# Kernel tuning notes

Hardware: AMD Instinct MI355X
Metric: run time of the kernel (lower is better)

## Reference

```python
import jax, jax.numpy as jnp
import numpy as np
import math

NUM_HEADS = 16
ROPE_BASE = 10000.0
SLIDING_WINDOW = 512  # note: original triu-then-tril composition makes the mask empty (no-op)


def _rope_cos_sin(seq_len, head_dim, dtype):
    inv_freq = 1.0 / (ROPE_BASE ** (jnp.arange(0, head_dim, 2, dtype=jnp.float32) / head_dim))
    t = jnp.arange(seq_len, dtype=jnp.float32)
    freqs = t[:, None] * inv_freq[None, :]          # [S, D/2]
    emb = jnp.concatenate([freqs, freqs], axis=-1)  # [S, D]
    # reshape to broadcast over [B, S, H, D]
    return jnp.cos(emb)[None, :, None, :].astype(dtype), jnp.sin(emb)[None, :, None, :].astype(dtype)


def _rotate_half(x):
    x1, x2 = jnp.split(x, 2, axis=-1)
    return jnp.concatenate([-x2, x1], axis=-1)


def setup_inputs() -> dict:
    key = jax.random.key(0)
    ks = jax.random.split(key, 9)
    B, S, E = 2, 2048, 2048
    sc = 1.0 / math.sqrt(E)
    return {
        "hidden_states": jax.random.normal(ks[0], (B, S, E), dtype=jnp.float32),
        "Wq": jax.random.normal(ks[1], (E, E), dtype=jnp.float32) * sc,
        "bq": jax.random.normal(ks[2], (E,), dtype=jnp.float32) * 0.01,
        "Wk": jax.random.normal(ks[3], (E, E), dtype=jnp.float32) * sc,
        "bk": jax.random.normal(ks[4], (E,), dtype=jnp.float32) * 0.01,
        "Wv": jax.random.normal(ks[5], (E, E), dtype=jnp.float32) * sc,
        "bv": jax.random.normal(ks[6], (E,), dtype=jnp.float32) * 0.01,
        "Wo": jax.random.normal(ks[7], (E, E), dtype=jnp.float32) * sc,
        "bo": jax.random.normal(ks[8], (E,), dtype=jnp.float32) * 0.01,
    }


def reference(hidden_states, Wq, bq, Wk, bk, Wv, bv, Wo, bo):
    B, S, E = hidden_states.shape
    H = NUM_HEADS
    D = E // H
    q = (hidden_states @ Wq.T + bq).reshape(B, S, H, D)
    k = (hidden_states @ Wk.T + bk).reshape(B, S, H, D)
    v = (hidden_states @ Wv.T + bv).reshape(B, S, H, D)

    cos, sin = _rope_cos_sin(S, D, q.dtype)
    q = q * cos + _rotate_half(q) * sin
    k = k * cos + _rotate_half(k) * sin

    scale = 1.0 / math.sqrt(D)
    scores = jnp.einsum("bqhd,bkhd->bhqk", q, k) * scale  # [B,H,S,S]
    # Faithful to source: triu(ones, +w) followed by tril(..., -w) is empty -> mask is a no-op.
    attn = jax.nn.softmax(scores, axis=-1)
    out = jnp.einsum("bhqk,bkhd->bqhd", attn, v).reshape(B, S, E)
    return out @ Wo.T + bo
```

## Files before the change

kernel.cpp:

```cpp
#include <hip/hip_runtime.h>
#include <hip/hip_bf16.h>

#define B_ 2
#define S_ 2048
#define E_ 2048
#define H_ 16
#define D_ 128
#define M_ (B_*S_)
#define NQKV_ (3*E_)

typedef __attribute__((ext_vector_type(8))) short bf16x8;
typedef __attribute__((ext_vector_type(4))) float f32x4;
typedef __attribute__((ext_vector_type(4))) unsigned short u16x4;
typedef __attribute__((ext_vector_type(2))) unsigned u32x2;

__device__ __forceinline__ unsigned short f2bf(float f) {
  union { float f; unsigned u; } v; v.f = f;
  unsigned r = v.u + 0x7fffu + ((v.u >> 16) & 1u);
  return (unsigned short)(r >> 16);
}
__device__ __forceinline__ float bf2f(unsigned short h) {
  union { unsigned u; float f; } v; v.u = ((unsigned)h) << 16;
  return v.f;
}

__device__ __forceinline__ void gload_lds16(const void* g, void* l) {
  __builtin_amdgcn_global_load_lds(
      (const __attribute__((address_space(1))) unsigned*)g,
      (__attribute__((address_space(3))) unsigned*)l, 16, 0, 0);
}

__global__ __launch_bounds__(256) void prep_kernel(
    const float* __restrict__ hs,
    const float* __restrict__ Wq, const float* __restrict__ Wk, const float* __restrict__ Wv,
    const float* __restrict__ Wo,
    const float* __restrict__ bq, const float* __restrict__ bk, const float* __restrict__ bv,
    unsigned short* __restrict__ hsb, unsigned short* __restrict__ Wqkv,
    unsigned short* __restrict__ Wob, float* __restrict__ biasqkv,
    float* __restrict__ cosT, float* __restrict__ sinT)
{
  const int seg = blockIdx.y;
  const int t0 = blockIdx.x * 256 + threadIdx.x;
  const int stride = gridDim.x * 256;
  if (seg == 0) {
    const int n = (M_*E_)/4;
    for (int i = t0; i < n; i += stride) {
      f32x4 v = ((const f32x4*)hs)[i];
      u16x4 o; o[0]=f2bf(v[0]); o[1]=f2bf(v[1]); o[2]=f2bf(v[2]); o[3]=f2bf(v[3]);
      ((u16x4*)hsb)[i] = o;
    }
  } else if (seg == 1) {
    const int n = (3*E_*E_)/4;
    for (int i = t0; i < n; i += stride) {
      int e4 = i << 2;
      int r = e4 >> 11;
      int k = e4 & 2047;
      const float* src = (r < E_) ? (Wq + ((size_t)r << 11) + k)
                       : (r < 2*E_) ? (Wk + ((size_t)(r - E_) << 11) + k)
                       : (Wv + ((size_t)(r - 2*E_) << 11) + k);
      f32x4 v = *(const f32x4*)src;
      u16x4 o; o[0]=f2bf(v[0]); o[1]=f2bf(v[1]); o[2]=f2bf(v[2]); o[3]=f2bf(v[3]);
      ((u16x4*)Wqkv)[i] = o;
    }
  } else if (seg == 2) {
    const int n = (E_*E_)/4;
    for (int i = t0; i < n; i += stride) {
      f32x4 v = ((const f32x4*)Wo)[i];
      u16x4 o; o[0]=f2bf(v[0]); o[1]=f2bf(v[1]); o[2]=f2bf(v[2]); o[3]=f2bf(v[3]);
      ((u16x4*)Wob)[i] = o;
    }
  } else if (seg == 3) {
    for (int i = t0; i < NQKV_; i += stride)
      biasqkv[i] = (i < E_) ? bq[i] : (i < 2*E_) ? bk[i - E_] : bv[i - 2*E_];
  } else {
    for (int i = t0; i < S_*64; i += stride) {
      int j = i & 63, s = i >> 6;
      float inv = exp2f(-(float)j * (13.287712379549449f / 64.0f));
      float ang = (float)s * inv;
      cosT[i] = cosf(ang);
      sinT[i] = sinf(ang);
    }
  }
}

#define STGA(BUFP, TKT, KS) do { \
    unsigned short* dst_ = lds + (BUFP)*24576 + (KS)*4096; \
    const unsigned short* src_ = Abase + (TKT)*64 + (KS)*32; \
    int cc_ = tid; int row_ = cc_ >> 2, c2_ = cc_ & 3; \
    int sc_ = c2_ ^ ((row_ >> 1) & 3); \
    gload_lds16(src_ + (size_t)row_*K + sc_*8, (char*)dst_ + cc_*16); \
  } while(0)

#define STGB(BUFP, TKT, KS) do { \
    unsigned short* dst_ = lds + (BUFP)*24576 + 8192 + (KS)*8192; \
    const unsigned short* src_ = Bbase + (TKT)*64 + (KS)*32; \
    _Pragma("unroll") \
    for (int j_ = 0; j_ < 2; ++j_) { \
      int cc_ = (j_ << 9) + tid; int row_ = cc_ >> 2, c2_ = cc_ & 3; \
      int sc_ = c2_ ^ ((row_ >> 1) & 3); \
      gload_lds16(src_ + (size_t)row_*K + sc_*8, (char*)dst_ + cc_*16); \
    } } while(0)

#define PHA(KS, BUF, ISSUE, WAITV) do { \
    { const unsigned short* Ab_ = lds + (BUF)*24576 + (KS)*4096; \
      _Pragma("unroll") \
      for (int j_ = 0; j_ < 4; ++j_) { \
        int row_ = wr*64 + j_*16 + l15; \
        af[j_] = *(const bf16x8*)(Ab_ + row_*32 + ((l4 ^ ((row_>>1)&3)) << 3)); } \
      const unsigned short* Bb_ = lds + (BUF)*24576 + 8192 + (KS)*8192; \
      _Pragma("unroll") \
      for (int j_ = 0; j_ < 4; ++j_) { \
        int row_ = wc*64 + j_*16 + l15; \
        bf[j_] = *(const bf16x8*)(Bb_ + row_*32 + ((l4 ^ ((row_>>1)&3)) << 3)); } } \
    ISSUE; \
    __builtin_amdgcn_sched_barrier(0); \
    __builtin_amdgcn_s_barrier(); \
    asm volatile("s_waitcnt lgkmcnt(0)" ::: "memory"); \
    __builtin_amdgcn_sched_barrier(0); \
    __builtin_amdgcn_s_setprio(1); \
    _Pragma("unroll") \
    for (int mm_ = 0; mm_ < 4; ++mm_) \
      _Pragma("unroll") \
      for (int nn_ = 0; nn_ < 4; ++nn_) \
        acc[mm_][nn_] = __builtin_amdgcn_mfma_f32_16x16x32_bf16(af[mm_], bf[nn_], acc[mm_][nn_], 0,0,0); \
    __builtin_amdgcn_s_setprio(0); \
    WAITV; \
    __builtin_amdgcn_s_barrier(); \
  } while(0)

template<int OUT_F32>
__global__ __launch_bounds__(512, 2) void gemmA(
    const unsigned short* __restrict__ A,
    const unsigned short* __restrict__ Bm,
    const float* __restrict__ bias,
    void* __restrict__ Cv,
    int M, int N, int K)
{
  __shared__ __align__(16) unsigned short lds[73728];
  const int tid = threadIdx.x;
  const int lane = tid & 63;
  const int w = tid >> 6;
  const int wr = w >> 2, wc = w & 3;
  const int l15 = lane & 15, l4 = lane >> 4;

  const int ntile = N >> 8;
  int wg = blockIdx.x;
  const int cpx = gridDim.x >> 3;
  wg = (wg & 7) * cpx + (wg >> 3);
  const int tm = wg / ntile, tn = wg % ntile;

  const unsigned short* Abase = A + ((size_t)tm*128)*K;
  const unsigned short* Bbase = Bm + ((size_t)tn*256)*K;

  f32x4 acc[4][4] = {};
  bf16x8 af[4], bf[4];

  const int NT = K >> 6;

  STGA(0,0,0); STGB(0,0,0); STGA(0,0,1); STGB(0,0,1);
  STGA(1,1,0); STGB(1,1,0); STGA(1,1,1); STGB(1,1,1);
  __builtin_amdgcn_sched_barrier(0);
  asm volatile("s_waitcnt vmcnt(6)" ::: "memory");
  __builtin_amdgcn_s_barrier();
  __builtin_amdgcn_sched_barrier(0);

  int bufc = 0, bufn = 2;
  for (int i = 0; i < NT; ++i) {
    const bool st = (i + 2 < NT);
    const bool more = (i + 1 < NT);
    PHA(0, bufc, if (st) { STGA(bufn, i+2, 0); STGB(bufn, i+2, 0); }, );
    PHA(1, bufc, if (st) { STGA(bufn, i+2, 1); STGB(bufn, i+2, 1); },
        if (st) { asm volatile("s_waitcnt vmcnt(6)" ::: "memory"); }
        else if (more) { asm volatile("s_waitcnt vmcnt(0)" ::: "memory"); });
    bufc = (bufc + 1 == 3) ? 0 : bufc + 1;
    bufn = (bufn + 1 == 3) ? 0 : bufn + 1;
  }

  #pragma unroll
  for (int mt = 0; mt < 4; ++mt) {
    #pragma unroll
    for (int nt = 0; nt < 4; ++nt) {
      int colg = tn*256 + wc*64 + nt*16 + l15;
      float bvv = bias[colg];
      #pragma unroll
      for (int r = 0; r < 4; ++r) {
        int rowg = tm*128 + wr*64 + mt*16 + l4*4 + r;
        float v = acc[mt][nt][r] + bvv;
        if (OUT_F32) ((float*)Cv)[(size_t)rowg*N + colg] = v;
        else ((unsigned short*)Cv)[(size_t)rowg*N + colg] = f2bf(v);
      }
    }
  }
}

__global__ __launch_bounds__(256) void rope_kernel(
    unsigned short* __restrict__ qkv, const float* __restrict__ cosT, const float* __restrict__ sinT)
{
  int t = blockIdx.x*256 + threadIdx.x;
  int i  = t & 63;
  int h  = (t >> 6) & 15;
  int m  = t >> 10;
  int s  = m & (S_-1);
  float c = cosT[s*64 + i], sn = sinT[s*64 + i];
  const float scale = 0.08838834764831845f * 1.4426950408889634f;
  size_t base = (size_t)m*NQKV_ + h*128;
  float q1 = bf2f(qkv[base+i]), q2 = bf2f(qkv[base+64+i]);
  qkv[base+i]    = f2bf((q1*c - q2*sn)*scale);
  qkv[base+64+i] = f2bf((q2*c + q1*sn)*scale);
  size_t kb = base + E_;
  float k1 = bf2f(qkv[kb+i]), k2 = bf2f(qkv[kb+64+i]);
  qkv[kb+i]    = f2bf(k1*c - k2*sn);
  qkv[kb+64+i] = f2bf(k2*c + k1*sn);
}

__global__ __launch_bounds__(256) void transv_kernel(
    const unsigned short* __restrict__ qkv, unsigned short* __restrict__ Vt)
{
  __shared__ unsigned short t[32][33];
  int bid = blockIdx.x;
  int st = bid & 63;
  int dt = (bid >> 6) & 3;
  int bh = bid >> 8;
  int b = bh >> 4, h = bh & 15;
  int tx = threadIdx.x & 31, ty = threadIdx.x >> 5;
  #pragma unroll
  for (int j = 0; j < 4; ++j) {
    int r = ty + j*8;
    t[r][tx] = qkv[(size_t)(b*S_ + st*32 + r)*NQKV_ + 2*E_ + h*128 + dt*32 + tx];
  }
  __syncthreads();
  #pragma unroll
  for (int j = 0; j < 4; ++j) {
    int r = ty + j*8;
    Vt[((size_t)bh*D_ + dt*32 + r)*S_ + st*32 + tx] = t[tx][r];
  }
}

__global__ __launch_bounds__(256, 2) void attn_kernel(
    const unsigned short* __restrict__ qkv, const unsigned short* __restrict__ Vt,
    unsigned short* __restrict__ Ao)
{
  __shared__ unsigned short lK[64*128];
  __shared__ unsigned short lV[128*64];
  __shared__ __align__(16) unsigned short lP[4*32*64];
  int bid = blockIdx.x;
  bid = (bid & 7)*64 + (bid >> 3);
  const int qt = bid & 15;
  const int bh = bid >> 4;
  const int b = bh >> 4, h = bh & 15;
  const int tid = threadIdx.x, lane = tid & 63, w = tid >> 6;
  const int l15 = lane & 15, l4 = lane >> 4;

  bf16x8 qf[2][4];
  #pragma unroll
  for (int g = 0; g < 2; ++g) {
    const int qrow = qt*128 + w*32 + g*16 + l15;
    const unsigned short* qp = qkv + (size_t)(b*S_ + qrow)*NQKV_ + h*128 + l4*8;
    #pragma unroll
    for (int f = 0; f < 4; ++f) qf[g][f] = *(const bf16x8*)(qp + f*32);
  }

  f32x4 O[2][8];
  #pragma unroll
  for (int g = 0; g < 2; ++g)
    #pragma unroll
    for (int i = 0; i < 8; ++i) O[g][i] = (f32x4){0.f,0.f,0.f,0.f};
  float mx[2] = {-1e30f,-1e30f}, lsum[2] = {0.f,0.f};

  unsigned short* myP = lP + w*(32*64);
  const int ksw = (l15 & 7) << 3;
  const size_t kbase = (size_t)b*S_*NQKV_ + E_ + (size_t)h*128;
  const size_t vbase = (size_t)bh*D_*S_;

  for (int kt = 0; kt < S_; kt += 64) {
    #pragma unroll
    for (int i = 0; i < 4; ++i) {
      int cc = i*256 + tid;
      int row = cc >> 4, col = cc & 15;
      int scol = col ^ (row & 7);
      gload_lds16(qkv + kbase + (size_t)(kt + row)*NQKV_ + scol*8, (char*)lK + cc*16);
    }
    #pragma unroll
    for (int i = 0; i < 4; ++i) {
      int cc = i*256 + tid;
      int row = cc >> 3, col = cc & 7;
      int scol = col ^ ((row & 7) ^ ((row >> 3) & 7));
      gload_lds16(Vt + vbase + (size_t)row*S_ + kt + scol*8, (char*)lV + cc*16);
    }
    asm volatile("s_waitcnt vmcnt(0)" ::: "memory");
    __syncthreads();

    f32x4 sfr[2][4];
    #pragma unroll
    for (int nf = 0; nf < 4; ++nf) {
      f32x4 s0 = (f32x4){0.f,0.f,0.f,0.f};
      f32x4 s1 = (f32x4){0.f,0.f,0.f,0.f};
      #pragma unroll
      for (int ks = 0; ks < 4; ++ks) {
        int row = nf*16 + l15;
        int ch = (ks*4 + l4) ^ (row & 7);
        bf16x8 kf = *(const bf16x8*)(lK + row*128 + ch*8);
        s0 = __builtin_amdgcn_mfma_f32_16x16x32_bf16(kf, qf[0][ks], s0, 0, 0, 0);
        s1 = __builtin_amdgcn_mfma_f32_16x16x32_bf16(kf, qf[1][ks], s1, 0, 0, 0);
      }
      sfr[0][nf] = s0; sfr[1][nf] = s1;
    }

    float vm[2];
    #pragma unroll
    for (int g = 0; g < 2; ++g) {
      float v = -1e30f;
      #pragma unroll
      for (int nf = 0; nf < 4; ++nf)
        #pragma unroll
        for (int r = 0; r < 4; ++r) v = fmaxf(v, sfr[g][nf][r]);
      v = fmaxf(v, __shfl_xor(v, 16, 64));
      v = fmaxf(v, __shfl_xor(v, 32, 64));
      vm[g] = v;
    }

    if (__any((vm[0] > mx[0] + 8.0f) || (vm[1] > mx[1] + 8.0f))) {
      #pragma unroll
      for (int g = 0; g < 2; ++g) {
        float mn = fmaxf(mx[g], vm[g]);
        float al = __builtin_amdgcn_exp2f(mx[g] - mn);
        mx[g] = mn;
        lsum[g] *= al;
        #pragma unroll
        for (int r = 0; r < 4; ++r) {
          float ar = __shfl(al, (lane & 48) + l4*4 + r, 64);
          #pragma unroll
          for (int df = 0; df < 8; ++df) O[g][df][r] *= ar;
        }
      }
    }

    #pragma unroll
    for (int g = 0; g < 2; ++g) {
      float ps = 0.f;
      #pragma unroll
      for (int nf = 0; nf < 4; ++nf) {
        #pragma unroll
        for (int r = 0; r < 4; ++r) {
          float p = __builtin_amdgcn_exp2f(sfr[g][nf][r] - mx[g]);
          sfr[g][nf][r] = p;
          ps += p;
        }
      }
      ps += __shfl_xor(ps, 16, 64);
      ps += __shfl_xor(ps, 32, 64);
      lsum[g] += ps;
    }

    #pragma unroll
    for (int g = 0; g < 2; ++g) {
      #pragma unroll
      for (int nf = 0; nf < 4; ++nf) {
        unsigned lo = (unsigned)f2bf(sfr[g][nf][0]) | ((unsigned)f2bf(sfr[g][nf][1]) << 16);
        unsigned hi = (unsigned)f2bf(sfr[g][nf][2]) | ((unsigned)f2bf(sfr[g][nf][3]) << 16);
        int k0 = (nf*16 + l4*4) ^ ksw;
        u32x2 val; val[0] = lo; val[1] = hi;
        *(u32x2*)(myP + (g*16 + l15)*64 + k0) = val;
      }
    }
    asm volatile("s_waitcnt lgkmcnt(0)" ::: "memory");

    #pragma unroll
    for (int ks2 = 0; ks2 < 2; ++ks2) {
      int kk = (ks2*32 + l4*8) ^ ksw;
      bf16x8 pf0 = *(const bf16x8*)(myP + l15*64 + kk);
      bf16x8 pf1 = *(const bf16x8*)(myP + (16 + l15)*64 + kk);
      #pragma unroll
      for (int df = 0; df < 8; ++df) {
        int row = df*16 + l15;
        int ch = (ks2*4 + l4) ^ ((row & 7) ^ ((row >> 3) & 7));
        bf16x8 vf = *(const bf16x8*)(lV + row*64 + ch*8);
        O[0][df] = __builtin_amdgcn_mfma_f32_16x16x32_bf16(pf0, vf, O[0][df], 0, 0, 0);
        O[1][df] = __builtin_amdgcn_mfma_f32_16x16x32_bf16(pf1, vf, O[1][df], 0, 0, 0);
      }
    }
    __syncthreads();
  }

  #pragma unroll
  for (int g = 0; g < 2; ++g) {
    float linv = 1.0f / lsum[g];
    float inv[4];
    #pragma unroll
    for (int r = 0; r < 4; ++r) inv[r] = __shfl(linv, (lane & 48) + l4*4 + r, 64);
    #pragma unroll
    for (int df = 0; df < 8; ++df) {
      int colg = h*128 + df*16 + l15;
      #pragma unroll
      for (int r = 0; r < 4; ++r) {
        int rowg = qt*128 + w*32 + g*16 + l4*4 + r;
        Ao[(size_t)(b*S_ + rowg)*E_ + colg] = f2bf(O[g][df][r] * inv[r]);
      }
    }
  }
}

extern "C" void kernel_launch(void* const* d_in, const int* in_sizes, int n_in,
                              void* d_out, int out_size, void* d_ws, size_t ws_size,
                              hipStream_t stream) {
  const float* hs = (const float*)d_in[0];
  const float* Wq = (const float*)d_in[1];
  const float* bq = (const float*)d_in[2];
  const float* Wk = (const float*)d_in[3];
  const float* bk = (const float*)d_in[4];
  const float* Wv = (const float*)d_in[5];
  const float* bv = (const float*)d_in[6];
  const float* Wo = (const float*)d_in[7];
  const float* bo = (const float*)d_in[8];
  float* out = (float*)d_out;

  char* p = (char*)d_ws;
  auto alloc = [&](size_t bytes) { char* r = p; p += (bytes + 255) & ~(size_t)255; return r; };
  unsigned short* hsb  = (unsigned short*)alloc((size_t)M_*E_*2);
  unsigned short* Wqkv = (unsigned short*)alloc((size_t)NQKV_*E_*2);
  unsigned short* Wob  = (unsigned short*)alloc((size_t)E_*E_*2);
  unsigned short* qkv  = (unsigned short*)alloc((size_t)M_*NQKV_*2);
  unsigned short* Vt   = (unsigned short*)alloc((size_t)B_*H_*D_*S_*2);
  unsigned short* Ao   = (unsigned short*)alloc((size_t)M_*E_*2);
  float* biasqkv = (float*)alloc((size_t)NQKV_*4);
  float* cosT = (float*)alloc((size_t)S_*64*4);
  float* sinT = (float*)alloc((size_t)S_*64*4);

  prep_kernel<<<dim3(2048, 5), 256, 0, stream>>>(hs, Wq, Wk, Wv, Wo, bq, bk, bv,
      hsb, Wqkv, Wob, biasqkv, cosT, sinT);
  gemmA<0><<<dim3((M_/128)*(NQKV_/256)), 512, 0, stream>>>(hsb, Wqkv, biasqkv, qkv, M_, NQKV_, E_);
  rope_kernel<<<dim3((M_*H_*64)/256), 256, 0, stream>>>(qkv, cosT, sinT);
  transv_kernel<<<dim3(B_*H_*(D_/32)*(S_/32)), 256, 0, stream>>>(qkv, Vt);
  attn_kernel<<<dim3(B_*H_*(S_/128)), 256, 0, stream>>>(qkv, Vt, Ao);
  gemmA<1><<<dim3((M_/128)*(E_/256)), 512, 0, stream>>>(Ao, Wob, bo, out, M_, E_, E_);
}
```

Baseline: 298.7 us.

## Add 256x256-tile GEMM for Q/K projection and split V projection

Adds a new GEMM kernel with 256x256 output tiles (each wave computing 128x64) and a double-buffered two-stage K pipeline. It is used for the Q and K projection columns. The V projection goes through the existing 128x256 kernel, called with a separate leading dimension so both write into the shared qkv buffer. Larger tiles raise arithmetic intensity and data reuse per block, but they double accumulator registers, cut the block count to 128 for Q/K, and add an extra kernel launch.

```diff
diff --git a/kernel.cpp b/kernel.cpp
--- a/kernel.cpp
+++ b/kernel.cpp
@@ -79,6 +79,123 @@
       float ang = (float)s * inv;
       cosT[i] = cosf(ang);
       sinT[i] = sinf(ang);
+    }
+  }
+}
+
+#define STAGE8(basePtr, BUF, AB, KS, KT) do { \
+    unsigned short* dst_ = lds + (BUF)*32768 + (AB)*16384 + (KS)*8192; \
+    const unsigned short* src_ = (basePtr) + (KT)*64 + (KS)*32; \
+    _Pragma("unroll") \
+    for (int j_ = 0; j_ < 2; ++j_) { \
+      int cc_ = (j_ << 9) + tid; \
+      int row_ = cc_ >> 2, c2_ = cc_ & 3; \
+      int sc_ = c2_ ^ ((row_ >> 1) & 3); \
+      gload_lds16(src_ + (size_t)row_*K + sc_*8, (char*)dst_ + cc_*16); \
+    } } while(0)
+
+#define LOADA8(MH, KS, BUF) do { \
+    const unsigned short* Ab_ = lds + (BUF)*32768 + (KS)*8192; \
+    _Pragma("unroll") \
+    for (int j_ = 0; j_ < 4; ++j_) { \
+      int row_ = wr*128 + ((MH)*4 + j_)*16 + l15; \
+      af[j_] = *(const bf16x8*)(Ab_ + row_*32 + ((l4 ^ ((row_>>1)&3)) << 3)); \
+    } } while(0)
+
+#define LOADB8(KS, BUF) do { \
+    const unsigned short* Bb_ = lds + (BUF)*32768 + 16384 + (KS)*8192; \
+    _Pragma("unroll") \
+    for (int j_ = 0; j_ < 4; ++j_) { \
+      int row_ = wc*64 + j_*16 + l15; \
+      bf[j_] = *(const bf16x8*)(Bb_ + row_*32 + ((l4 ^ ((row_>>1)&3)) << 3)); \
+    } } while(0)
+
+#define MFMAQ(MH) do { \
+    _Pragma("unroll") \
+    for (int mm_ = 0; mm_ < 4; ++mm_) \
+      _Pragma("unroll") \
+      for (int nn_ = 0; nn_ < 4; ++nn_) \
+        acc[(MH)*4+mm_][nn_] = __builtin_amdgcn_mfma_f32_16x16x32_bf16(af[mm_], bf[nn_], acc[(MH)*4+mm_][nn_], 0,0,0); \
+  } while(0)
+
+#define WVM6 asm volatile("s_waitcnt vmcnt(6)" ::: "memory")
+#define WVM0 asm volatile("s_waitcnt vmcnt(0)" ::: "memory")
+
+#define PHASE(MH, KS, BUF, ISSUE, WAITV) do { \
+    LOADA8(MH, KS, BUF); \
+    if ((MH) == 0) LOADB8(KS, BUF); \
+    ISSUE; \
+    __builtin_amdgcn_sched_barrier(0); \
+    __builtin_amdgcn_s_barrier(); \
+    asm volatile("s_waitcnt lgkmcnt(0)" ::: "memory"); \
+    __builtin_amdgcn_sched_barrier(0); \
+    __builtin_amdgcn_s_setprio(1); \
+    MFMAQ(MH); \
+    __builtin_amdgcn_s_setprio(0); \
+    WAITV; \
+    __builtin_amdgcn_s_barrier(); \
+  } while(0)
+
+__global__ __launch_bounds__(512, 2) void gemm8(
+    const unsigned short* __restrict__ A,
+    const unsigned short* __restrict__ Bm,
+    const float* __restrict__ bias,
+    unsigned short* __restrict__ Cv,
+    int M, int N, int K, int ldc)
+{
+  __shared__ __align__(16) unsigned short lds[65536];
+  const int tid = threadIdx.x;
+  const int lane = tid & 63;
+  const int w = tid >> 6;
+  const int wr = w >> 2, wc = w & 3;
+  const int l15 = lane & 15, l4 = lane >> 4;
+
+  const int ntile = N >> 8;
+  int wg = blockIdx.x;
+  const int cpx = gridDim.x >> 3;
+  wg = (wg & 7) * cpx + (wg >> 3);
+  const int tm = wg / ntile, tn = wg % ntile;
+
+  const unsigned short* Abase = A + ((size_t)tm*256)*K;
+  const unsigned short* Bbase = Bm + ((size_t)tn*256)*K;
+
+  f32x4 acc[8][4] = {};
+  bf16x8 af[4], bf[4];
+
+  const int NITER = K >> 7;
+
+  STAGE8(Bbase, 0, 1, 0, 0); STAGE8(Abase, 0, 0, 0, 0);
+  STAGE8(Bbase, 0, 1, 1, 0); STAGE8(Abase, 0, 0, 1, 0);
+  STAGE8(Bbase, 1, 1, 0, 1); STAGE8(Abase, 1, 0, 0, 1);
+  STAGE8(Bbase, 1, 1, 1, 1);
+  __builtin_amdgcn_sched_barrier(0);
+  WVM6;
+  __builtin_amdgcn_s_barrier();
+
+  for (int i = 0; i < NITER; ++i) {
+    const int t1k = 2*i + 1, t2k = 2*i + 2, t3k = 2*i + 3;
+    const bool nl = (i < NITER - 1);
+    PHASE(0, 0, 0, STAGE8(Abase, 1, 0, 1, t1k), );
+    PHASE(1, 0, 0, if (nl) STAGE8(Bbase, 0, 1, 0, t2k), );
+    PHASE(0, 1, 0, if (nl) STAGE8(Abase, 0, 0, 0, t2k), );
+    PHASE(1, 1, 0, if (nl) STAGE8(Bbase, 0, 1, 1, t2k), if (nl) WVM6; else WVM0);
+    PHASE(0, 0, 1, if (nl) STAGE8(Abase, 0, 0, 1, t2k), );
+    PHASE(1, 0, 1, if (nl) STAGE8(Bbase, 1, 1, 0, t3k), );
+    PHASE(0, 1, 1, if (nl) STAGE8(Abase, 1, 0, 0, t3k), );
+    PHASE(1, 1, 1, if (nl) STAGE8(Bbase, 1, 1, 1, t3k), if (nl) WVM6);
+  }
+
+  #pragma unroll
+  for (int mt = 0; mt < 8; ++mt) {
+    #pragma unroll
+    for (int nt = 0; nt < 4; ++nt) {
+      int colg = tn*256 + wc*64 + nt*16 + l15;
+      float bvv = bias[colg];
+      #pragma unroll
+      for (int r = 0; r < 4; ++r) {
+        int rowg = tm*256 + wr*128 + mt*16 + l4*4 + r;
+        Cv[(size_t)rowg*ldc + colg] = f2bf(acc[mt][nt][r] + bvv);
+      }
     }
   }
 }
@@ -134,7 +251,7 @@
     const unsigned short* __restrict__ Bm,
     const float* __restrict__ bias,
     void* __restrict__ Cv,
-    int M, int N, int K)
+    int M, int N, int K, int ldc)
 {
   __shared__ __align__(16) unsigned short lds[73728];
   const int tid = threadIdx.x;
@@ -186,8 +303,8 @@
       for (int r = 0; r < 4; ++r) {
         int rowg = tm*128 + wr*64 + mt*16 + l4*4 + r;
         float v = acc[mt][nt][r] + bvv;
-        if (OUT_F32) ((float*)Cv)[(size_t)rowg*N + colg] = v;
-        else ((unsigned short*)Cv)[(size_t)rowg*N + colg] = f2bf(v);
+        if (OUT_F32) ((float*)Cv)[(size_t)rowg*ldc + colg] = v;
+        else ((unsigned short*)Cv)[(size_t)rowg*ldc + colg] = f2bf(v);
       }
     }
   }
@@ -428,9 +545,13 @@
 
   prep_kernel<<<dim3(2048, 5), 256, 0, stream>>>(hs, Wq, Wk, Wv, Wo, bq, bk, bv,
       hsb, Wqkv, Wob, biasqkv, cosT, sinT);
-  gemmA<0><<<dim3((M_/128)*(NQKV_/256)), 512, 0, stream>>>(hsb, Wqkv, biasqkv, qkv, M_, NQKV_, E_);
+  gemm8<<<dim3((M_/256)*(2*E_/256)), 512, 0, stream>>>(
+      hsb, Wqkv, biasqkv, qkv, M_, 2*E_, E_, NQKV_);
+  gemmA<0><<<dim3((M_/128)*(E_/256)), 512, 0, stream>>>(
+      hsb, Wqkv + (size_t)2*E_*E_, biasqkv + 2*E_, qkv + 2*E_, M_, E_, E_, NQKV_);
   rope_kernel<<<dim3((M_*H_*64)/256), 256, 0, stream>>>(qkv, cosT, sinT);
   transv_kernel<<<dim3(B_*H_*(D_/32)*(S_/32)), 256, 0, stream>>>(qkv, Vt);
   attn_kernel<<<dim3(B_*H_*(S_/128)), 256, 0, stream>>>(qkv, Vt, Ao);
-  gemmA<1><<<dim3((M_/128)*(E_/256)), 512, 0, stream>>>(Ao, Wob, bo, out, M_, E_, E_);
-}
+  gemmA<1><<<dim3((M_/128)*(E_/256)), 512, 0, stream>>>(
+      Ao, Wob, bo, out, M_, E_, E_, E_);
+}
```

After: 278.9 us. 6.6% less time.
